# Kernel optimization log

Hardware: AMD Instinct MI355X
Metric: run time of the kernel (lower is better)

Reference implementation:

```python
import jax, jax.numpy as jnp
import numpy as np

M, K, N, G = 64, 4096, 11008, 128  # tokens, infeatures, outfeatures, group_size
NUM_GROUPS = K // G  # 32


def _fp8_round_trip(w):
    # Simulate FP8 E4M3 storage of the quantized weight codes.
    return w.astype(jnp.float8_e4m3fn).astype(jnp.float32)


def setup_inputs() -> dict:
    key = jax.random.key(0)
    k1, k2, k3, k4 = jax.random.split(key, 4)
    x = jax.random.normal(k1, (M, K), dtype=jnp.float32)
    # FP8-representable weight codes (post round-trip, stored as f32 values)
    weight = _fp8_round_trip(jax.random.normal(k2, (N, K), dtype=jnp.float32) * 2.0)
    # Per-(out_feature, group) dequant scales, strictly positive
    weight_scale = jax.random.uniform(k3, (N, NUM_GROUPS), dtype=jnp.float32,
                                      minval=0.005, maxval=0.02)
    bias = jax.random.normal(k4, (N,), dtype=jnp.float32)
    return {"x": x, "weight": weight, "weight_scale": weight_scale, "bias": bias}


def reference(x, weight, weight_scale, bias):
    # Dequantize: each group of `G` consecutive in-features of an output row
    # shares one scale -> w_deq[o, i] = weight[o, i] * scale[o, i // G]
    n, k = weight.shape
    g = k // weight_scale.shape[1]
    w_deq = (weight.reshape(n, -1, g) * weight_scale[:, :, None]).reshape(n, k)
    # Fused dequant-matmul: out[m, o] = sum_i x[m, i] * w_deq[o, i] + bias[o]
    out = jnp.einsum("mk,nk->mn", x, w_deq) + bias
    return out
```

## Files before the change

### kernel.cpp

```cpp
#include <hip/hip_runtime.h>


#define Md 64
#define Kd 4096
#define Nd 11008
#define NGROUPS 32
#define BN 64
#define KSPLIT 8
#define KCHUNK (Kd / KSPLIT)
#define NGRP (KCHUNK / 128)
#define KBC (KCHUNK / 32)

typedef __attribute__((ext_vector_type(8))) __bf16 bf16x8;
typedef __attribute__((ext_vector_type(4))) float f32x4;


__global__ __launch_bounds__(256)
void xprep(const float* __restrict__ x, __bf16* __restrict__ xf)
{
    const int tid  = blockIdx.x * 256 + threadIdx.x;
    const int lane = tid & 63;
    const int t    = (tid >> 6) & 3;
    const int kb   = tid >> 8;
    const int row  = t * 16 + (lane & 15);
    const int col  = kb * 32 + (lane >> 4) * 8;
    const float4 a = *(const float4*)(x + (size_t)row * Kd + col);
    const float4 b = *(const float4*)(x + (size_t)row * Kd + col + 4);
    bf16x8 v = {(__bf16)a.x, (__bf16)a.y, (__bf16)a.z, (__bf16)a.w,
                (__bf16)b.x, (__bf16)b.y, (__bf16)b.z, (__bf16)b.w};
    *(bf16x8*)(xf + (size_t)tid * 8) = v;
}

__global__ __launch_bounds__(256, 4)
void qlinear_pass1(const float* __restrict__ w,
                   const __bf16* __restrict__ xf,
                   const float* __restrict__ scale,
                   float* __restrict__ ws)
{
    const int tid  = threadIdx.x;
    const int wv   = tid >> 6;
    const int lane = tid & 63;
    const int quad = lane >> 4;
    const int ln   = lane & 15;

    const int n0 = blockIdx.x * BN;
    const int ky = blockIdx.y;
    const int k0 = ky * KCHUNK;

    const int nrow = n0 + wv * 16 + ln;
    const float* wp = w + (size_t)nrow * Kd + k0 + quad * 8;

    const __bf16* xp = xf + (size_t)ky * KBC * 4 * 512 + lane * 8;

    float4 sc4 = *(const float4*)(scale + (size_t)nrow * NGROUPS + ky * NGRP);
    const float sc[4] = {sc4.x, sc4.y, sc4.z, sc4.w};

    f32x4 acc[4];
    #pragma unroll
    for (int t = 0; t < 4; ++t) acc[t] = (f32x4){0.f, 0.f, 0.f, 0.f};

    #pragma unroll
    for (int g = 0; g < NGRP; ++g) {
        f32x4 pg[4];
        #pragma unroll
        for (int t = 0; t < 4; ++t) pg[t] = (f32x4){0.f, 0.f, 0.f, 0.f};

        #pragma unroll
        for (int s = 0; s < 4; ++s) {
            const int kb = g * 4 + s;
            float4 wa = *(const float4*)(wp + kb * 32);
            float4 wb = *(const float4*)(wp + kb * 32 + 4);
            bf16x8 wf = {(__bf16)wa.x, (__bf16)wa.y, (__bf16)wa.z, (__bf16)wa.w,
                         (__bf16)wb.x, (__bf16)wb.y, (__bf16)wb.z, (__bf16)wb.w};
            #pragma unroll
            for (int t = 0; t < 4; ++t) {
                bf16x8 xv = *(const bf16x8*)(xp + ((size_t)kb * 4 + t) * 512);
                pg[t] = __builtin_amdgcn_mfma_f32_16x16x32_bf16(xv, wf, pg[t],
                                                                0, 0, 0);
            }
        }

        const float s = sc[g];
        #pragma unroll
        for (int t = 0; t < 4; ++t)
            #pragma unroll
            for (int r = 0; r < 4; ++r)
                acc[t][r] += s * pg[t][r];
    }

    float* op = ws + ((size_t)ky * Md) * Nd + n0 + wv * 16 + ln;
    #pragma unroll
    for (int t = 0; t < 4; ++t)
        #pragma unroll
        for (int r = 0; r < 4; ++r)
            op[(size_t)(t * 16 + quad * 4 + r) * Nd] = acc[t][r];
}

__global__ __launch_bounds__(256)
void qlinear_reduce(const float* __restrict__ ws,
                    const float* __restrict__ bias,
                    float* __restrict__ out)
{
    const int i4 = blockIdx.x * 256 + threadIdx.x;
    if (i4 >= (Md * Nd) / 4) return;
    const int n = (i4 * 4) % Nd;
    float4 v = *(const float4*)(bias + n);
    #pragma unroll
    for (int ky = 0; ky < KSPLIT; ++ky) {
        float4 p = *(const float4*)(ws + (size_t)ky * Md * Nd + (size_t)i4 * 4);
        v.x += p.x; v.y += p.y; v.z += p.z; v.w += p.w;
    }
    *(float4*)(out + (size_t)i4 * 4) = v;
}

extern "C" void kernel_launch(void* const* d_in, const int* in_sizes, int n_in,
                              void* d_out, int out_size, void* d_ws, size_t ws_size,
                              hipStream_t stream) {
    const float* x     = (const float*)d_in[0];
    const float* w     = (const float*)d_in[1];
    const float* scale = (const float*)d_in[2];
    const float* bias  = (const float*)d_in[3];
    float* out = (float*)d_out;
    float* ws  = (float*)d_ws;

    __bf16* xf = (__bf16*)(ws + (size_t)KSPLIT * Md * Nd);

    xprep<<<128, 256, 0, stream>>>(x, xf);

    dim3 grid1(Nd / BN, KSPLIT);
    qlinear_pass1<<<grid1, 256, 0, stream>>>(w, xf, scale, ws);

    qlinear_reduce<<<(Md * Nd / 4 + 255) / 256, 256, 0, stream>>>(ws, bias, out);
}
```

Measured before the change: 279.6 us.

## Stage weight tiles through double-buffered LDS with async global-to-LDS loads

Weight rows are now fetched with global_load_lds into a double-buffered, XOR-swizzled shared-memory tile. The next 64-column stage is prefetched while MFMAs run on the current one. The aim is to replace strided per-thread global loads with coalesced 16-byte row loads and to overlap memory traffic with compute. In exchange it adds a block barrier every stage and 32KB of LDS per block, which may cut occupancy below the requested 4 blocks per CU.

```diff
diff --git a/kernel.cpp b/kernel.cpp
--- a/kernel.cpp
+++ b/kernel.cpp
@@ -8,12 +8,12 @@
 #define BN 64
 #define KSPLIT 8
 #define KCHUNK (Kd / KSPLIT)
+#define NSTAGE (KCHUNK / 64)
 #define NGRP (KCHUNK / 128)
 #define KBC (KCHUNK / 32)
 
 typedef __attribute__((ext_vector_type(8))) __bf16 bf16x8;
 typedef __attribute__((ext_vector_type(4))) float f32x4;
-
 
 __global__ __launch_bounds__(256)
 void xprep(const float* __restrict__ x, __bf16* __restrict__ xf)
@@ -47,17 +47,36 @@
     const int ky = blockIdx.y;
     const int k0 = ky * KCHUNK;
 
+    __shared__ alignas(16) float lds_w[2][BN * 64];
+
+    const float* src[4];
+    #pragma unroll
+    for (int j = 0; j < 4; ++j) {
+        const int r   = wv * 16 + j * 4 + quad;
+        const int c16 = ln ^ (r & 7);
+        src[j] = w + (size_t)(n0 + r) * Kd + k0 + c16 * 4;
+    }
+
+    const __bf16* xp = xf + (size_t)ky * KBC * 4 * 512 + (size_t)lane * 8;
+
     const int nrow = n0 + wv * 16 + ln;
-    const float* wp = w + (size_t)nrow * Kd + k0 + quad * 8;
-
-    const __bf16* xp = xf + (size_t)ky * KBC * 4 * 512 + lane * 8;
-
     float4 sc4 = *(const float4*)(scale + (size_t)nrow * NGROUPS + ky * NGRP);
     const float sc[4] = {sc4.x, sc4.y, sc4.z, sc4.w};
+
+    const int rr = wv * 16 + ln;
+    const int rx = rr & 7;
 
     f32x4 acc[4];
     #pragma unroll
     for (int t = 0; t < 4; ++t) acc[t] = (f32x4){0.f, 0.f, 0.f, 0.f};
+
+    #pragma unroll
+    for (int j = 0; j < 4; ++j)
+        __builtin_amdgcn_global_load_lds(
+            (const __attribute__((address_space(1))) void*)src[j],
+            (__attribute__((address_space(3))) void*)&lds_w[0][(wv * 4 + j) * 256],
+            16, 0, 0);
+    __syncthreads();
 
     #pragma unroll
     for (int g = 0; g < NGRP; ++g) {
@@ -66,18 +85,38 @@
         for (int t = 0; t < 4; ++t) pg[t] = (f32x4){0.f, 0.f, 0.f, 0.f};
 
         #pragma unroll
-        for (int s = 0; s < 4; ++s) {
-            const int kb = g * 4 + s;
-            float4 wa = *(const float4*)(wp + kb * 32);
-            float4 wb = *(const float4*)(wp + kb * 32 + 4);
-            bf16x8 wf = {(__bf16)wa.x, (__bf16)wa.y, (__bf16)wa.z, (__bf16)wa.w,
-                         (__bf16)wb.x, (__bf16)wb.y, (__bf16)wb.z, (__bf16)wb.w};
+        for (int half = 0; half < 2; ++half) {
+            const int s   = g * 2 + half;
+            const int buf = s & 1;
+
+            if (s + 1 < NSTAGE) {
+                #pragma unroll
+                for (int j = 0; j < 4; ++j)
+                    __builtin_amdgcn_global_load_lds(
+                        (const __attribute__((address_space(1))) void*)(src[j] + (s + 1) * 64),
+                        (__attribute__((address_space(3))) void*)&lds_w[buf ^ 1][(wv * 4 + j) * 256],
+                        16, 0, 0);
+            }
+
             #pragma unroll
-            for (int t = 0; t < 4; ++t) {
-                bf16x8 xv = *(const bf16x8*)(xp + ((size_t)kb * 4 + t) * 512);
-                pg[t] = __builtin_amdgcn_mfma_f32_16x16x32_bf16(xv, wf, pg[t],
-                                                                0, 0, 0);
+            for (int ks = 0; ks < 2; ++ks) {
+                const int kb = s * 2 + ks;
+                bf16x8 xv[4];
+                #pragma unroll
+                for (int t = 0; t < 4; ++t)
+                    xv[t] = *(const bf16x8*)(xp + ((size_t)kb * 4 + t) * 512);
+
+                const int c0 = ks * 8 + quad * 2;
+                f32x4 fa = *(const f32x4*)&lds_w[buf][rr * 64 + (((c0    ) ^ rx) << 2)];
+                f32x4 fb = *(const f32x4*)&lds_w[buf][rr * 64 + (((c0 + 1) ^ rx) << 2)];
+                bf16x8 wf = {(__bf16)fa.x, (__bf16)fa.y, (__bf16)fa.z, (__bf16)fa.w,
+                             (__bf16)fb.x, (__bf16)fb.y, (__bf16)fb.z, (__bf16)fb.w};
+                #pragma unroll
+                for (int t = 0; t < 4; ++t)
+                    pg[t] = __builtin_amdgcn_mfma_f32_16x16x32_bf16(xv[t], wf, pg[t],
+                                                                    0, 0, 0);
             }
+            __syncthreads();
         }
 
         const float s = sc[g];
```

Measured after the change: 273.8 us. 2.1% less time.
